# Kernel tuning notes

Measured on AMD Instinct MI355X. Metric: run time of the kernel, lower is better.

## Reference

```python
import jax, jax.numpy as jnp
import numpy as np

N, C, H, W = 128, 3, 256, 256


def setup_inputs() -> dict:
    key = jax.random.key(0)
    k1, k2 = jax.random.split(key)
    inputs = jax.random.normal(k1, (N, C, H, W), dtype=jnp.float32)
    u = jax.random.uniform(k2, (N, 4), dtype=jnp.float32)
    # realistic crop params: scales in (0.3, 1.0], translations in (-0.2, 0.2)
    whbias = jnp.concatenate([0.3 + 0.7 * u[:, :2], 0.4 * u[:, 2:] - 0.2], axis=1)
    return {"inputs": inputs, "whbias": whbias}


def _reflect_clip(x, size):
    # PyTorch grid_sample padding_mode='reflection', align_corners=False:
    # reflect unnormalized coords about [-0.5, size-0.5], then clip to [0, size-1]
    span = float(size)
    x = jnp.abs(x + 0.5) % (2.0 * span)
    x = jnp.where(x > span, 2.0 * span - x, x) - 0.5
    return jnp.clip(x, 0.0, size - 1.0)


def _resized_crop(inputs, whbias):
    n, c, h, w = inputs.shape
    dt = inputs.dtype
    # F.affine_grid base coords, align_corners=False: centers of pixels in [-1, 1]
    xs = (jnp.arange(w, dtype=dt) + 0.5) * (2.0 / w) - 1.0  # [W]
    ys = (jnp.arange(h, dtype=dt) + 0.5) * (2.0 / h) - 1.0  # [H]
    w_s, h_s, w_b, h_b = whbias[:, 0], whbias[:, 1], whbias[:, 2], whbias[:, 3]
    # theta is diagonal + translation -> grid separable in x and y
    gx = w_s[:, None, None] * xs[None, None, :] + w_b[:, None, None]  # [N,H,W]
    gy = h_s[:, None, None] * ys[None, :, None] + h_b[:, None, None]  # [N,H,W]
    # unnormalize (align_corners=False): ix = ((gx+1)*W - 1)/2
    ix = _reflect_clip(((gx + 1.0) * w - 1.0) * 0.5, w)
    iy = _reflect_clip(((gy + 1.0) * h - 1.0) * 0.5, h)
    ix0 = jnp.floor(ix)
    iy0 = jnp.floor(iy)
    wx = (ix - ix0)[:, None]  # [N,1,H,W]
    wy = (iy - iy0)[:, None]
    ix0i = jnp.clip(ix0.astype(jnp.int32), 0, w - 1)
    ix1i = jnp.clip(ix0i + 1, 0, w - 1)
    iy0i = jnp.clip(iy0.astype(jnp.int32), 0, h - 1)
    iy1i = jnp.clip(iy0i + 1, 0, h - 1)

    def gather(img, yy, xx):  # img [C,H,W], yy/xx [H,W] -> [C,H,W]
        return img[:, yy, xx]

    g = jax.vmap(gather)
    v00 = g(inputs, iy0i, ix0i)
    v01 = g(inputs, iy0i, ix1i)
    v10 = g(inputs, iy1i, ix0i)
    v11 = g(inputs, iy1i, ix1i)
    # bilinear blend
    return (v00 * (1.0 - wx) * (1.0 - wy) + v01 * wx * (1.0 - wy)
            + v10 * (1.0 - wx) * wy + v11 * wx * wy)


def reference(inputs, whbias):
    # size=None -> no adaptive_avg_pool2d; output is [N,C,H,W]
    return _resized_crop(inputs, whbias)
```

## Files before the change

### kernel.cpp

```cpp
#include <hip/hip_runtime.h>


constexpr int N_ = 128, C_ = 3, H_ = 256, W_ = 256, HW_ = H_ * W_;
constexpr int ROWS_ = 9;
constexpr int LDSF_ = C_ * ROWS_ * W_;

__device__ __forceinline__ void coord(float scale, float bias, float xf, int size,
                                      int& i0, int& i1, float& w) {
    const float span = (float)size;
    const float two  = 2.0f * span;
    float xs  = (xf + 0.5f) * (2.0f / span) - 1.0f;
    float g   = scale * xs + bias;
    float pre = ((g + 1.0f) * span - 1.0f) * 0.5f;
    float t = fabsf(pre + 0.5f);
    t = t - two * floorf(t * (1.0f / two));
    t = (t > span) ? (two - t) : t;
    t -= 0.5f;
    t = fminf(fmaxf(t, 0.0f), span - 1.0f);
    float f = floorf(t);
    w  = t - f;
    i0 = (int)f;
    i1 = min(i0 + 1, size - 1);
}

__global__ __launch_bounds__(256)
void rrc_kernel(const float* __restrict__ in, const float* __restrict__ wh,
                float* __restrict__ out) {
    __shared__ float lds[LDSF_];
    const int n   = blockIdx.x >> 5;
    const int ys  = (blockIdx.x & 31) * 8;
    const int tid = threadIdx.x;
    const int xq  = tid & 63;
    const int yl  = tid >> 6;

    const float w_s = wh[n * 4 + 0];
    const float h_s = wh[n * 4 + 1];
    const float w_b = wh[n * 4 + 2];
    const float h_b = wh[n * 4 + 3];

    int rmin = H_ - 1, rmax = 0;
    int my0a = 0, my1a = 0, my0b = 0, my1b = 0;
    float wya = 0.0f, wyb = 0.0f;
#pragma unroll
    for (int r = 0; r < 8; ++r) {
        int a, b; float w;
        coord(h_s, h_b, (float)(ys + r), H_, a, b, w);
        rmin = min(rmin, a);
        rmax = max(rmax, b);
        if (r == yl)     { my0a = a; my1a = b; wya = w; }
        if (r == yl + 4) { my0b = a; my1b = b; wyb = w; }
    }
    const int nrows = rmax - rmin + 1;

    const float* __restrict__ inN = in + (size_t)n * C_ * HW_;
#pragma unroll
    for (int c = 0; c < C_; ++c) {
        for (int r = yl; r < nrows; r += 4) {
            const float4 v = *reinterpret_cast<const float4*>(
                inN + c * HW_ + (rmin + r) * W_ + xq * 4);
            *reinterpret_cast<float4*>(&lds[(c * ROWS_ + r) * W_ + xq * 4]) = v;
        }
    }
    __syncthreads();

    int ix0[4], ix1[4]; float wx[4];
#pragma unroll
    for (int j = 0; j < 4; ++j)
        coord(w_s, w_b, (float)(xq * 4 + j), W_, ix0[j], ix1[j], wx[j]);

    float* __restrict__ outN = out + (size_t)n * C_ * HW_;

#pragma unroll
    for (int g = 0; g < 2; ++g) {
        const int y  = ys + g * 4 + yl;
        const int b0 = ((g ? my0b : my0a) - rmin) * W_;
        const int b1 = ((g ? my1b : my1a) - rmin) * W_;
        const float wyr = g ? wyb : wya;
#pragma unroll
        for (int c = 0; c < C_; ++c) {
            const int co = c * ROWS_ * W_;
            float4 o; float* op = &o.x;
#pragma unroll
            for (int j = 0; j < 4; ++j) {
                const float v00 = lds[co + b0 + ix0[j]];
                const float v01 = lds[co + b0 + ix1[j]];
                const float v10 = lds[co + b1 + ix0[j]];
                const float v11 = lds[co + b1 + ix1[j]];
                const float top = v00 + wx[j] * (v01 - v00);
                const float bot = v10 + wx[j] * (v11 - v10);
                op[j] = top + wyr * (bot - top);
            }
            *reinterpret_cast<float4*>(outN + (c * H_ + y) * W_ + xq * 4) = o;
        }
    }
}

extern "C" void kernel_launch(void* const* d_in, const int* in_sizes, int n_in,
                              void* d_out, int out_size, void* d_ws, size_t ws_size,
                              hipStream_t stream) {
    const float* in = (const float*)d_in[0];
    const float* wh = (const float*)d_in[1];
    float* out      = (float*)d_out;
    (void)in_sizes; (void)n_in; (void)out_size; (void)d_ws; (void)ws_size;

    dim3 grid(N_ * 32);
    dim3 block(256);
    rrc_kernel<<<grid, block, 0, stream>>>(in, wh, out);
}
```

Baseline: 35.04 us.

## Halve rows per block, use nontemporal stores and derive x+1 neighbor

```diff
diff --git a/kernel.cpp b/kernel.cpp
--- a/kernel.cpp
+++ b/kernel.cpp
@@ -2,8 +2,10 @@
 
 
 constexpr int N_ = 128, C_ = 3, H_ = 256, W_ = 256, HW_ = H_ * W_;
-constexpr int ROWS_ = 9;
-constexpr int LDSF_ = C_ * ROWS_ * W_;
+constexpr int ROWS_ = 5;
+constexpr int LDSF_ = C_ * ROWS_ * W_ + 4;
+
+typedef float f32x4 __attribute__((ext_vector_type(4)));
 
 __device__ __forceinline__ void coord(float scale, float bias, float xf, int size,
                                       int& i0, int& i1, float& w) {
@@ -23,12 +25,12 @@
     i1 = min(i0 + 1, size - 1);
 }
 
-__global__ __launch_bounds__(256)
+__global__ __launch_bounds__(256, 8)
 void rrc_kernel(const float* __restrict__ in, const float* __restrict__ wh,
                 float* __restrict__ out) {
     __shared__ float lds[LDSF_];
-    const int n   = blockIdx.x >> 5;
-    const int ys  = (blockIdx.x & 31) * 8;
+    const int n   = blockIdx.x >> 6;
+    const int ys  = (blockIdx.x & 63) * 4;
     const int tid = threadIdx.x;
     const int xq  = tid & 63;
     const int yl  = tid >> 6;
@@ -39,16 +41,14 @@
     const float h_b = wh[n * 4 + 3];
 
     int rmin = H_ - 1, rmax = 0;
-    int my0a = 0, my1a = 0, my0b = 0, my1b = 0;
-    float wya = 0.0f, wyb = 0.0f;
+    int my0 = 0;  float wy = 0.0f;
 #pragma unroll
-    for (int r = 0; r < 8; ++r) {
+    for (int r = 0; r < 4; ++r) {
         int a, b; float w;
         coord(h_s, h_b, (float)(ys + r), H_, a, b, w);
         rmin = min(rmin, a);
         rmax = max(rmax, b);
-        if (r == yl)     { my0a = a; my1a = b; wya = w; }
-        if (r == yl + 4) { my0b = a; my1b = b; wyb = w; }
+        if (r == yl) { my0 = a; wy = w; }
     }
     const int nrows = rmax - rmin + 1;
 
@@ -56,42 +56,44 @@
 #pragma unroll
     for (int c = 0; c < C_; ++c) {
         for (int r = yl; r < nrows; r += 4) {
-            const float4 v = *reinterpret_cast<const float4*>(
+            const f32x4 v = *reinterpret_cast<const f32x4*>(
                 inN + c * HW_ + (rmin + r) * W_ + xq * 4);
-            *reinterpret_cast<float4*>(&lds[(c * ROWS_ + r) * W_ + xq * 4]) = v;
+            *reinterpret_cast<f32x4*>(&lds[(c * ROWS_ + r) * W_ + xq * 4]) = v;
         }
     }
     __syncthreads();
 
-    int ix0[4], ix1[4]; float wx[4];
+    int ix0[4]; float wx[4];
 #pragma unroll
-    for (int j = 0; j < 4; ++j)
-        coord(w_s, w_b, (float)(xq * 4 + j), W_, ix0[j], ix1[j], wx[j]);
+    for (int j = 0; j < 4; ++j) {
+        int i1_unused;
+        coord(w_s, w_b, (float)(xq * 4 + j), W_, ix0[j], i1_unused, wx[j]);
+    }
 
     float* __restrict__ outN = out + (size_t)n * C_ * HW_;
 
+    const int y  = ys + yl;
+    const int b0 = (my0 - rmin) * W_;
+    const int b1 = min(my0 + 1, H_ - 1) >= rmax ? (rmax - rmin) * W_
+                                                : (my0 + 1 - rmin) * W_;
 #pragma unroll
-    for (int g = 0; g < 2; ++g) {
-        const int y  = ys + g * 4 + yl;
-        const int b0 = ((g ? my0b : my0a) - rmin) * W_;
-        const int b1 = ((g ? my1b : my1a) - rmin) * W_;
-        const float wyr = g ? wyb : wya;
+    for (int c = 0; c < C_; ++c) {
+        const int co = c * ROWS_ * W_;
+        f32x4 o;
 #pragma unroll
-        for (int c = 0; c < C_; ++c) {
-            const int co = c * ROWS_ * W_;
-            float4 o; float* op = &o.x;
-#pragma unroll
-            for (int j = 0; j < 4; ++j) {
-                const float v00 = lds[co + b0 + ix0[j]];
-                const float v01 = lds[co + b0 + ix1[j]];
-                const float v10 = lds[co + b1 + ix0[j]];
-                const float v11 = lds[co + b1 + ix1[j]];
-                const float top = v00 + wx[j] * (v01 - v00);
-                const float bot = v10 + wx[j] * (v11 - v10);
-                op[j] = top + wyr * (bot - top);
-            }
-            *reinterpret_cast<float4*>(outN + (c * H_ + y) * W_ + xq * 4) = o;
+        for (int j = 0; j < 4; ++j) {
+            const int a0 = co + b0 + ix0[j];
+            const int a1 = co + b1 + ix0[j];
+            const float v00 = lds[a0];
+            const float v01 = lds[a0 + 1];
+            const float v10 = lds[a1];
+            const float v11 = lds[a1 + 1];
+            const float top = v00 + wx[j] * (v01 - v00);
+            const float bot = v10 + wx[j] * (v11 - v10);
+            o[j] = top + wy * (bot - top);
         }
+        __builtin_nontemporal_store(o, reinterpret_cast<f32x4*>(
+            outN + (c * H_ + y) * W_ + xq * 4));
     }
 }
 
@@ -103,7 +105,7 @@
     float* out      = (float*)d_out;
     (void)in_sizes; (void)n_in; (void)out_size; (void)d_ws; (void)ws_size;
 
-    dim3 grid(N_ * 32);
+    dim3 grid(N_ * 64);
     dim3 block(256);
     rrc_kernel<<<grid, block, 0, stream>>>(in, wh, out);
 }
```

Result: no change. 35.39 us (+1.0%).
